# Kernel optimization log

Measured on AMD Instinct MI355X. Metric: run time of the kernel, lower is better.

Reference implementation:

```python
import jax, jax.numpy as jnp
import numpy as np

SIGMA = 1.0

def _pairwise_sqdist(x, y):
    # x: [N,3], y: [M,3] -> [N,M] squared distances via gram expansion
    xx = jnp.sum(x * x, axis=-1)[:, None]
    yy = jnp.sum(y * y, axis=-1)[None, :]
    xy = x @ y.T
    return jnp.maximum(xx + yy - 2.0 * xy, 0.0)

def _cauchy(d2, sigma):
    return 1.0 / (1.0 + d2 / (sigma * sigma))

def setup_inputs() -> dict:
    key = jax.random.key(0)
    k1, k2, k3, k4 = jax.random.split(key, 4)
    V, N, M = 4096, 8192, 8192
    src_vertices = jax.random.normal(k1, (V, 3), dtype=jnp.float32)
    tar_normals = jax.random.normal(k2, (M, 3), dtype=jnp.float32)
    tar_centers = jax.random.normal(k3, (M, 3), dtype=jnp.float32)
    src_indices = jax.random.randint(k4, (N, 3), 0, V)
    return {"src_vertices": src_vertices, "tar_normals": tar_normals,
            "tar_centers": tar_centers, "src_indices": src_indices}

def reference(src_vertices, tar_normals, tar_centers, src_indices):
    # Gather triangle vertices: [N,3(verts),3(xyz)]
    tris = src_vertices[src_indices]
    a, b, c = tris[:, 0, :], tris[:, 1, :], tris[:, 2, :]
    normals = 0.5 * jnp.cross(a - b, c - b)        # [N,3]
    centers = tris.sum(axis=1) / 3.0               # [N,3]

    # Currents energy with cauchy kernel K(x,y) = 1/(1 + |x-y|^2/sigma^2)
    K_ss = _cauchy(_pairwise_sqdist(centers, centers), SIGMA)      # [N,N]
    K_st = _cauchy(_pairwise_sqdist(centers, tar_centers), SIGMA)  # [N,M]
    K_tt = _cauchy(_pairwise_sqdist(tar_centers, tar_centers), SIGMA)  # [M,M]

    e_ss = jnp.sum(K_ss * (normals @ normals.T))
    e_st = jnp.sum(K_st * (normals @ tar_normals.T))
    e_tt = jnp.sum(K_tt * (tar_normals @ tar_normals.T))
    return e_ss - 2.0 * e_st + e_tt
```

## Files before the change

kernel.cpp:

```cpp
#include <hip/hip_runtime.h>

typedef short bf16x8 __attribute__((ext_vector_type(8)));
typedef float f32x16 __attribute__((ext_vector_type(16)));

static __device__ __forceinline__ unsigned short f2bf(float x) {
    unsigned u = __builtin_bit_cast(unsigned, x);
    unsigned r = (u + 0x7FFFu + ((u >> 16) & 1u)) >> 16;
    return (unsigned short)r;
}
static __device__ __forceinline__ float bf2f(unsigned short h) {
    unsigned u = (unsigned)h << 16;
    return __builtin_bit_cast(float, u);
}


__global__ void dc_pack(const float* __restrict__ verts,
                        const float* __restrict__ tnorm,
                        const float* __restrict__ tcent,
                        const int* __restrict__ idx,
                        unsigned short* __restrict__ ws,
                        float* __restrict__ out,
                        int N, int M) {
    int p = blockIdx.x * blockDim.x + threadIdx.x;
    if (p == 0) out[0] = 0.0f;
    int P = N + M;
    if (p >= P) return;

    float cx, cy, cz, nx, ny, nz;
    if (p < N) {
        int i0 = idx[3 * p + 0], i1 = idx[3 * p + 1], i2 = idx[3 * p + 2];
        float ax = verts[3 * i0], ay = verts[3 * i0 + 1], az = verts[3 * i0 + 2];
        float bx = verts[3 * i1], by = verts[3 * i1 + 1], bz = verts[3 * i1 + 2];
        float qx = verts[3 * i2], qy = verts[3 * i2 + 1], qz = verts[3 * i2 + 2];
        float ux = ax - bx, uy = ay - by, uz = az - bz;
        float vx = qx - bx, vy = qy - by, vz = qz - bz;
        nx = 0.5f * (uy * vz - uz * vy);
        ny = 0.5f * (uz * vx - ux * vz);
        nz = 0.5f * (ux * vy - uy * vx);
        cx = (ax + bx + qx) * (1.0f / 3.0f);
        cy = (ay + by + qy) * (1.0f / 3.0f);
        cz = (az + bz + qz) * (1.0f / 3.0f);
    } else {
        int t = p - N;
        cx = tcent[3 * t]; cy = tcent[3 * t + 1]; cz = tcent[3 * t + 2];
        nx = -tnorm[3 * t]; ny = -tnorm[3 * t + 1]; nz = -tnorm[3 * t + 2];
    }

    unsigned short chx = f2bf(cx), chy = f2bf(cy), chz = f2bf(cz);
    unsigned short clx = f2bf(cx - bf2f(chx));
    unsigned short cly = f2bf(cy - bf2f(chy));
    unsigned short clz = f2bf(cz - bf2f(chz));
    unsigned short nhx = f2bf(nx), nhy = f2bf(ny), nhz = f2bf(nz);
    unsigned short nlx = f2bf(nx - bf2f(nhx));
    unsigned short nly = f2bf(ny - bf2f(nhy));
    unsigned short nlz = f2bf(nz - bf2f(nhz));
    float ex = bf2f(chx) + bf2f(clx);
    float ey = bf2f(chy) + bf2f(cly);
    float ez = bf2f(chz) + bf2f(clz);
    float s = ex * ex + ey * ey + ez * ez;
    unsigned short sh = f2bf(s), sl = f2bf(s - bf2f(sh));
    unsigned short m2hx = f2bf(-2.0f * bf2f(chx)), m2hy = f2bf(-2.0f * bf2f(chy)), m2hz = f2bf(-2.0f * bf2f(chz));
    unsigned short m2lx = f2bf(-2.0f * bf2f(clx)), m2ly = f2bf(-2.0f * bf2f(cly)), m2lz = f2bf(-2.0f * bf2f(clz));
    const unsigned short one = 0x3F80;

    __align__(16) unsigned short A1v[16] = {
        m2hx, m2hy, m2hz,  m2hx, m2hy, m2hz,  m2lx, m2ly, m2lz,
        sh, sl,  one, one,  one,  0, 0 };
    __align__(16) unsigned short B1v[16] = {
        chx, chy, chz,  clx, cly, clz,  chx, chy, chz,
        one, one,  sh, sl,  one,  0, 0 };
    __align__(16) unsigned short A2v[16] = {
        nhx, nhy, nhz,  nhx, nhy, nhz,  nlx, nly, nlz,
        0, 0, 0, 0, 0, 0, 0 };
    __align__(16) unsigned short B2v[16] = {
        nhx, nhy, nhz,  nlx, nly, nlz,  nhx, nhy, nhz,
        0, 0, 0, 0, 0, 0, 0 };

    size_t arr = (size_t)P * 16;
    unsigned short* A1 = ws;
    unsigned short* A2 = ws + arr;
    unsigned short* B1 = ws + 2 * arr;
    unsigned short* B2 = ws + 3 * arr;

    int tile = p >> 5, m = p & 31;
    size_t lo = ((size_t)tile * 64 + m) * 8;
    size_t hi = lo + 32 * 8;

    *(uint4*)(A1 + lo) = *(const uint4*)&A1v[0];
    *(uint4*)(A1 + hi) = *(const uint4*)&A1v[8];
    *(uint4*)(A2 + lo) = *(const uint4*)&A2v[0];
    *(uint4*)(A2 + hi) = *(const uint4*)&A2v[8];
    *(uint4*)(B1 + lo) = *(const uint4*)&B1v[0];
    *(uint4*)(B1 + hi) = *(const uint4*)&B1v[8];
    *(uint4*)(B2 + lo) = *(const uint4*)&B2v[0];
    *(uint4*)(B2 + hi) = *(const uint4*)&B2v[8];
}

static __device__ __forceinline__ void acc4(float4& part, const f32x16& d1, const f32x16& d2) {
#pragma unroll
    for (int g = 0; g < 4; ++g) {
        const int r = 4 * g;
        float p01 = d1[r] * d1[r + 1];
        float p23 = d1[r + 2] * d1[r + 3];
        float n01 = fmaf(d2[r], d1[r + 1], d2[r + 1] * d1[r]);
        float n23 = fmaf(d2[r + 2], d1[r + 3], d2[r + 3] * d1[r + 2]);
        float t   = p01 * p23;
        float num = fmaf(n01, p23, n23 * p01);
        (&part.x)[g] = fmaf(num, __builtin_amdgcn_rcpf(t), (&part.x)[g]);
    }
}

__global__ __launch_bounds__(256, 6) void dc_pair_mfma(
    const unsigned short* __restrict__ ws, float* __restrict__ out, int P) {
    __shared__ float wsum[4];

    const int nT = P >> 5;
    size_t arr = (size_t)P * 16;
    const unsigned short* A1 = ws;
    const unsigned short* A2 = ws + arr;
    const unsigned short* B1 = ws + 2 * arr;
    const unsigned short* B2 = ws + 3 * arr;

    int tid = threadIdx.x;
    int lane = tid & 63, wv = tid >> 6;
    int gi = blockIdx.x * 4 + wv;
    int rp = gi / 24, c = gi - 24 * rp;
    int I0 = 2 * rp, I1 = I0 + 1;

    int st  = (c < 16) ? (1 + 11 * c) : (177 + 10 * (c - 16));
    int len = (c < 16) ? 11 : 10;

    const size_t lo = (size_t)lane * 8;

    bf16x8 a1_0 = *(const bf16x8*)(A1 + (size_t)I0 * 512 + lo);
    bf16x8 a2_0 = *(const bf16x8*)(A2 + (size_t)I0 * 512 + lo);
    bf16x8 a1_1 = *(const bf16x8*)(A1 + (size_t)I1 * 512 + lo);
    bf16x8 a2_1 = *(const bf16x8*)(A2 + (size_t)I1 * 512 + lo);

    const f32x16 zero = {0.f,0.f,0.f,0.f,0.f,0.f,0.f,0.f,0.f,0.f,0.f,0.f,0.f,0.f,0.f,0.f};
    float4 partA = make_float4(0.f, 0.f, 0.f, 0.f);
    float4 corrP = make_float4(0.f, 0.f, 0.f, 0.f);
    float4 corrM = make_float4(0.f, 0.f, 0.f, 0.f);

    auto wrap = [&](int j) -> size_t {
        return (size_t)(j >= nT ? j - nT : j) * 512;
    };
    auto one_tile = [&](float4& part, const bf16x8& x1, const bf16x8& x2, int jm) {
        const bf16x8 b1 = *(const bf16x8*)(B1 + (size_t)jm * 512 + lo);
        const bf16x8 b2 = *(const bf16x8*)(B2 + (size_t)jm * 512 + lo);
        f32x16 d1 = __builtin_amdgcn_mfma_f32_32x32x16_bf16(x1, b1, zero, 0, 0, 0);
        f32x16 d2 = __builtin_amdgcn_mfma_f32_32x32x16_bf16(x2, b2, zero, 0, 0, 0);
        acc4(part, d1, d2);
    };

    int js = I0 + st;
#pragma unroll 1
    for (int it = 0; it < len; ++it) {
        size_t o = wrap(js + it);
        bf16x8 b1 = *(const bf16x8*)(B1 + o + lo);
        bf16x8 b2 = *(const bf16x8*)(B2 + o + lo);
        f32x16 d1 = __builtin_amdgcn_mfma_f32_32x32x16_bf16(a1_0, b1, zero, 0, 0, 0);
        f32x16 d2 = __builtin_amdgcn_mfma_f32_32x32x16_bf16(a2_0, b2, zero, 0, 0, 0);
        acc4(partA, d1, d2);
        f32x16 e1 = __builtin_amdgcn_mfma_f32_32x32x16_bf16(a1_1, b1, zero, 0, 0, 0);
        f32x16 e2 = __builtin_amdgcn_mfma_f32_32x32x16_bf16(a2_1, b2, zero, 0, 0, 0);
        acc4(partA, e1, e2);
    }

    if (c == 0) {
        one_tile(corrP, a1_0, a2_0, I0);
        one_tile(corrM, a1_1, a2_1, I0 + 1);
    } else if (c == 23) {
        int v = I0 + 256; if (v >= nT) v -= nT;
        int y = I0 + 257; if (y >= nT) y -= nT;
        one_tile(corrM, a1_0, a2_0, v);
        one_tile(corrP, a1_1, a2_1, y);
    }

    float s = 2.0f * (partA.x + partA.y + partA.z + partA.w)
            + (corrP.x + corrP.y + corrP.z + corrP.w)
            - (corrM.x + corrM.y + corrM.z + corrM.w);
#pragma unroll
    for (int off = 32; off > 0; off >>= 1) s += __shfl_down(s, off, 64);
    if (lane == 0) wsum[wv] = s;
    __syncthreads();
    if (tid == 0) {
        float t = wsum[0] + wsum[1] + wsum[2] + wsum[3];
        atomicAdd(out, t);
    }
}

extern "C" void kernel_launch(void* const* d_in, const int* in_sizes, int n_in,
                              void* d_out, int out_size, void* d_ws, size_t ws_size,
                              hipStream_t stream) {
    const float* verts = (const float*)d_in[0];
    const float* tnorm = (const float*)d_in[1];
    const float* tcent = (const float*)d_in[2];
    const int*   sidx  = (const int*)d_in[3];

    int M = in_sizes[1] / 3;
    int N = in_sizes[3] / 3;
    int P = N + M;

    unsigned short* ws = (unsigned short*)d_ws;
    float* out = (float*)d_out;

    int bblocks = (P + 255) / 256;
    dc_pack<<<bblocks, 256, 0, stream>>>(verts, tnorm, tcent, sidx, ws, out, N, M);

    dc_pair_mfma<<<1536, 256, 0, stream>>>(ws, out, P);
}
```

Measured before the change: 93.70 us.

## Stage B tiles into LDS with double-buffered async global-to-LDS loads

Reorganises the pair kernel so each block owns one row-pair and a quarter of the 256-tile band, with four waves sharing B tiles staged into shared memory through global_load_lds and a two-buffer pipeline. The goal is to overlap global loads with MFMA work and to stop each wave reissuing its own global B loads. In exchange it adds a block barrier per stage, lowers the launch-bounds occupancy hint, and shrinks the grid to 1024 blocks. The diagonal and wrap corrections are moved to wave 0 only.

```diff
diff --git a/kernel.cpp b/kernel.cpp
--- a/kernel.cpp
+++ b/kernel.cpp
@@ -2,6 +2,10 @@
 
 typedef short bf16x8 __attribute__((ext_vector_type(8)));
 typedef float f32x16 __attribute__((ext_vector_type(16)));
+
+#define GLOAD_LDS16(g, l) __builtin_amdgcn_global_load_lds(                    \
+    (const __attribute__((address_space(1))) unsigned int*)(g),                \
+    (__attribute__((address_space(3))) unsigned int*)(l), 16, 0, 0)
 
 static __device__ __forceinline__ unsigned short f2bf(float x) {
     unsigned u = __builtin_bit_cast(unsigned, x);
@@ -110,8 +114,9 @@
     }
 }
 
-__global__ __launch_bounds__(256, 6) void dc_pair_mfma(
+__global__ __launch_bounds__(256, 4) void dc_pair_mfma(
     const unsigned short* __restrict__ ws, float* __restrict__ out, int P) {
+    __shared__ unsigned short sB[2][8][1024];
     __shared__ float wsum[4];
 
     const int nT = P >> 5;
@@ -123,12 +128,9 @@
 
     int tid = threadIdx.x;
     int lane = tid & 63, wv = tid >> 6;
-    int gi = blockIdx.x * 4 + wv;
-    int rp = gi / 24, c = gi - 24 * rp;
+    int bx = blockIdx.x;
+    int rp = bx >> 2, c = bx & 3;
     int I0 = 2 * rp, I1 = I0 + 1;
-
-    int st  = (c < 16) ? (1 + 11 * c) : (177 + 10 * (c - 16));
-    int len = (c < 16) ? 11 : 10;
 
     const size_t lo = (size_t)lane * 8;
 
@@ -142,8 +144,27 @@
     float4 corrP = make_float4(0.f, 0.f, 0.f, 0.f);
     float4 corrM = make_float4(0.f, 0.f, 0.f, 0.f);
 
-    auto wrap = [&](int j) -> size_t {
-        return (size_t)(j >= nT ? j - nT : j) * 512;
+    auto stage = [&](int b, int bf) {
+#pragma unroll
+        for (int t = 0; t < 2; ++t) {
+            int slot = 2 * wv + t;
+            int j = I0 + 1 + 64 * c + 8 * b + slot;
+            if (j >= nT) j -= nT;
+            const unsigned short* g1 = B1 + (size_t)j * 512 + lo;
+            const unsigned short* g2 = B2 + (size_t)j * 512 + lo;
+            GLOAD_LDS16(g1, &sB[bf][slot][0]);
+            GLOAD_LDS16(g2, &sB[bf][slot][512]);
+        }
+    };
+    auto process_slot = [&](int bf, int s) {
+        const bf16x8 b1 = *(const bf16x8*)&sB[bf][s][lane * 8];
+        const bf16x8 b2 = *(const bf16x8*)&sB[bf][s][512 + lane * 8];
+        f32x16 d1 = __builtin_amdgcn_mfma_f32_32x32x16_bf16(a1_0, b1, zero, 0, 0, 0);
+        f32x16 d2 = __builtin_amdgcn_mfma_f32_32x32x16_bf16(a2_0, b2, zero, 0, 0, 0);
+        acc4(partA, d1, d2);
+        f32x16 e1 = __builtin_amdgcn_mfma_f32_32x32x16_bf16(a1_1, b1, zero, 0, 0, 0);
+        f32x16 e2 = __builtin_amdgcn_mfma_f32_32x32x16_bf16(a2_1, b2, zero, 0, 0, 0);
+        acc4(partA, e1, e2);
     };
     auto one_tile = [&](float4& part, const bf16x8& x1, const bf16x8& x2, int jm) {
         const bf16x8 b1 = *(const bf16x8*)(B1 + (size_t)jm * 512 + lo);
@@ -153,28 +174,27 @@
         acc4(part, d1, d2);
     };
 
-    int js = I0 + st;
+    stage(0, 0);
+    __syncthreads();
 #pragma unroll 1
-    for (int it = 0; it < len; ++it) {
-        size_t o = wrap(js + it);
-        bf16x8 b1 = *(const bf16x8*)(B1 + o + lo);
-        bf16x8 b2 = *(const bf16x8*)(B2 + o + lo);
-        f32x16 d1 = __builtin_amdgcn_mfma_f32_32x32x16_bf16(a1_0, b1, zero, 0, 0, 0);
-        f32x16 d2 = __builtin_amdgcn_mfma_f32_32x32x16_bf16(a2_0, b2, zero, 0, 0, 0);
-        acc4(partA, d1, d2);
-        f32x16 e1 = __builtin_amdgcn_mfma_f32_32x32x16_bf16(a1_1, b1, zero, 0, 0, 0);
-        f32x16 e2 = __builtin_amdgcn_mfma_f32_32x32x16_bf16(a2_1, b2, zero, 0, 0, 0);
-        acc4(partA, e1, e2);
-    }
-
-    if (c == 0) {
-        one_tile(corrP, a1_0, a2_0, I0);
-        one_tile(corrM, a1_1, a2_1, I0 + 1);
-    } else if (c == 23) {
-        int v = I0 + 256; if (v >= nT) v -= nT;
-        int y = I0 + 257; if (y >= nT) y -= nT;
-        one_tile(corrM, a1_0, a2_0, v);
-        one_tile(corrP, a1_1, a2_1, y);
+    for (int b = 0; b < 8; ++b) {
+        int bf = b & 1;
+        if (b < 7) stage(b + 1, bf ^ 1);
+        process_slot(bf, wv);
+        process_slot(bf, wv + 4);
+        __syncthreads();
+    }
+
+    if (wv == 0) {
+        if (c == 0) {
+            one_tile(corrP, a1_0, a2_0, I0);
+            one_tile(corrM, a1_1, a2_1, I0 + 1);
+        } else if (c == 3) {
+            int v = I0 + 256; if (v >= nT) v -= nT;
+            int y = I0 + 257; if (y >= nT) y -= nT;
+            one_tile(corrM, a1_0, a2_0, v);
+            one_tile(corrP, a1_1, a2_1, y);
+        }
     }
 
     float s = 2.0f * (partA.x + partA.y + partA.z + partA.w)
@@ -208,5 +228,5 @@
     int bblocks = (P + 255) / 256;
     dc_pack<<<bblocks, 256, 0, stream>>>(verts, tnorm, tcent, sidx, ws, out, N, M);
 
-    dc_pair_mfma<<<1536, 256, 0, stream>>>(ws, out, P);
-}
+    dc_pair_mfma<<<1024, 256, 0, stream>>>(ws, out, P);
+}
```

Measured after the change: 84.77 us. -9.5%, faster.
